# Kernel optimization log

Hardware: AMD Instinct MI355X
Metric: run time of the kernel (lower is better)

## Reference

```python
import jax, jax.numpy as jnp
import numpy as np

BN_EPS = 1e-5

def _batchnorm(x):
    # BatchNorm1d(affine=False) in training mode: per-feature batch stats, biased var
    m = jnp.mean(x, axis=0)
    v = jnp.var(x, axis=0)
    return (x - m) * jax.lax.rsqrt(v + BN_EPS)

def setup_inputs() -> dict:
    key = jax.random.key(0)
    ks = jax.random.split(key, 8)
    B, S, H, I = 2, 2048, 1024, 4096
    NE, NS, K = 16384, 128, 16
    return {
        "hidden_states": jax.random.normal(ks[0], (B, S, H), dtype=jnp.float32),
        "gate_w": jax.random.normal(ks[1], (I, H), dtype=jnp.float32) * 0.02,
        "up_w": jax.random.normal(ks[2], (I, H), dtype=jnp.float32) * 0.02,
        "down_w": jax.random.normal(ks[3], (H, I), dtype=jnp.float32) * 0.02,
        "router_x_w": jax.random.normal(ks[4], (NS, H), dtype=jnp.float32) * 0.02,
        "router_y_w": jax.random.normal(ks[5], (NS, H), dtype=jnp.float32) * 0.02,
        "up_embed": jax.random.normal(ks[6], (NE, H), dtype=jnp.float32) * 0.02,
        "down_embed": jax.random.normal(ks[7], (NE, H), dtype=jnp.float32) * 0.02,
        "top_k": K,
    }

def reference(hidden_states, gate_w, up_w, down_w, router_x_w, router_y_w, up_embed, down_embed, top_k):
    B, S, H = hidden_states.shape
    ns = router_x_w.shape[0]  # num_expert_sqrt
    x = hidden_states.reshape(-1, H)  # [N, H], N = B*S

    # product-key router: two grid log-softmaxes, outer-sum, global top-k
    lpx = jax.nn.log_softmax(_batchnorm(x @ router_x_w.T), axis=-1)  # [N, ns]
    lpy = jax.nn.log_softmax(_batchnorm(x @ router_y_w.T), axis=-1)  # [N, ns]
    all_scores = (lpx[:, :, None] + lpy[:, None, :]).reshape(-1, ns * ns)  # [N, ns^2]
    scores, indices = jax.lax.top_k(all_scores, top_k)  # [N, k]
    routing_weights = jnp.exp(scores)

    # per-token expert embedding gather + small bmm chain (PEER-style)
    ue = up_embed[indices]    # [N, k, H]
    de = down_embed[indices]  # [N, k, H]
    ew = jnp.einsum('nkh,nh->nk', ue, x)
    ew = jax.nn.silu(ew) * routing_weights
    experts_states = jnp.einsum('nk,nkh->nh', ew, de).reshape(B, S, H)

    # dense gated MLP
    dense = (jax.nn.silu(x @ gate_w.T) * (x @ up_w.T)) @ down_w.T
    return dense.reshape(B, S, H) + experts_states
```

## Files before the change

kernel.cpp:

```cpp
#include <hip/hip_runtime.h>

typedef float f32x4 __attribute__((ext_vector_type(4)));
typedef short bf16x8 __attribute__((ext_vector_type(8)));
typedef unsigned short u16;

#define NEG_INF (-1e30f)

__device__ __forceinline__ u16 f2bf(float f) {
    unsigned u = __builtin_bit_cast(unsigned, f);
    unsigned r = u + 0x7FFFu + ((u >> 16) & 1u);
    return (u16)(r >> 16);
}
__device__ __forceinline__ unsigned pk2(float a, float b) {
    unsigned r;
    asm("v_cvt_pk_bf16_f32 %0, %1, %2" : "=v"(r) : "v"(a), "v"(b));
    return r;
}

__device__ __forceinline__ float wave_max(float v) {
    #pragma unroll
    for (int o = 32; o > 0; o >>= 1) v = fmaxf(v, __shfl_xor(v, o, 64));
    return v;
}
__device__ __forceinline__ float wave_sum(float v) {
    #pragma unroll
    for (int o = 32; o > 0; o >>= 1) v += __shfl_xor(v, o, 64);
    return v;
}
__device__ __forceinline__ void wave_argmax(float& v, int& i) {
    #pragma unroll
    for (int o = 32; o > 0; o >>= 1) {
        float ov = __shfl_xor(v, o, 64);
        int oi = __shfl_xor(i, o, 64);
        if (ov > v || (ov == v && oi < i)) { v = ov; i = oi; }
    }
}

__device__ __forceinline__ void g2l16(const void* g, void* l) {
    __builtin_amdgcn_global_load_lds((__attribute__((address_space(1))) void*)g,
                                     (__attribute__((address_space(3))) void*)l,
                                     16, 0, 0);
}

template<int NROUND>
__device__ __forceinline__ void stage_bf16(const u16* __restrict__ src, int ld,
                                           u16* dst, int tid) {
    #pragma unroll
    for (int r = 0; r < NROUND; ++r) {
        int e = r * 2048 + tid * 8;
        int row = e >> 6, col = e & 63;
        g2l16(src + (size_t)row * ld + col, dst + e);
    }
}
template<int NROUND>
__device__ __forceinline__ void stage_f32(const float* __restrict__ src, int ld,
                                          u16* dst, int tid) {
    #pragma unroll
    for (int r = 0; r < NROUND; ++r) {
        int e = r * 2048 + tid * 8;
        int row = e >> 6, col = e & 63;
        const float* s = src + (size_t)row * ld + col;
        float4 a = *reinterpret_cast<const float4*>(s);
        float4 b = *reinterpret_cast<const float4*>(s + 4);
        uint4 pk;
        pk.x = pk2(a.x, a.y); pk.y = pk2(a.z, a.w);
        pk.z = pk2(b.x, b.y); pk.w = pk2(b.z, b.w);
        *reinterpret_cast<uint4*>(dst + e) = pk;
    }
}
__device__ __forceinline__ bf16x8 frag(const u16* lds, int row0, int ks, int lane) {
    return *reinterpret_cast<const bf16x8*>(
        lds + (row0 + (lane & 15)) * 64 + ks * 32 + (lane >> 4) * 8);
}

template<int NROUND>
__device__ __forceinline__ void stage32_bf16(const u16* __restrict__ src, int ld,
                                             u16* dst, int tid) {
    #pragma unroll
    for (int r = 0; r < NROUND; ++r) {
        int e = r * 2048 + tid * 8;
        int row = e >> 5, col = e & 31;
        g2l16(src + (size_t)row * ld + col, dst + e);
    }
}
template<int NROUND>
__device__ __forceinline__ void stage32_f32(const float* __restrict__ src, int ld,
                                            u16* dst, int tid) {
    #pragma unroll
    for (int r = 0; r < NROUND; ++r) {
        int e = r * 1024 + tid * 4;
        int row = e >> 5, col = e & 31;
        float4 v = *reinterpret_cast<const float4*>(src + (size_t)row * ld + col);
        uint2 pk;
        pk.x = pk2(v.x, v.y); pk.y = pk2(v.z, v.w);
        *reinterpret_cast<uint2*>(dst + e) = pk;
    }
}
__device__ __forceinline__ bf16x8 frag32(const u16* lds, int row0, int lane) {
    return *reinterpret_cast<const bf16x8*>(
        lds + (row0 + (lane & 15)) * 32 + (lane >> 4) * 8);
}

__global__ void conv_x(const float* __restrict__ s, u16* __restrict__ d) {
    size_t i = (size_t)blockIdx.x * 256 + threadIdx.x;
    float4 v = *reinterpret_cast<const float4*>(s + i * 4);
    uint2 pk;
    pk.x = pk2(v.x, v.y); pk.y = pk2(v.z, v.w);
    *reinterpret_cast<uint2*>(d + i * 4) = pk;
}

__global__ __launch_bounds__(256, 2) void gemm_router(
    const float* __restrict__ X, const float* __restrict__ RX, const float* __restrict__ RY,
    float* __restrict__ R) {
    __shared__ u16 As[8192];
    __shared__ u16 Bs[4096];
    int tid = threadIdx.x, lane = tid & 63, wave = tid >> 6;
    int rowBase = blockIdx.y * 128, colBase = blockIdx.x * 64;
    const float* Bp = (blockIdx.x < 2) ? RX + (size_t)colBase * 1024
                                       : RY + (size_t)(colBase - 128) * 1024;
    int wm = (wave >> 1) * 64, wn = (wave & 1) * 32;
    f32x4 acc[4][2] = {};
    for (int k0 = 0; k0 < 1024; k0 += 64) {
        stage_f32<4>(X + (size_t)rowBase * 1024 + k0, 1024, As, tid);
        stage_f32<2>(Bp + k0, 1024, Bs, tid);
        __syncthreads();
        #pragma unroll
        for (int ks = 0; ks < 2; ++ks) {
            bf16x8 af[4], bfr[2];
            #pragma unroll
            for (int i = 0; i < 4; ++i) af[i] = frag(As, wm + i * 16, ks, lane);
            #pragma unroll
            for (int j = 0; j < 2; ++j) bfr[j] = frag(Bs, wn + j * 16, ks, lane);
            #pragma unroll
            for (int i = 0; i < 4; ++i)
                #pragma unroll
                for (int j = 0; j < 2; ++j)
                    acc[i][j] = __builtin_amdgcn_mfma_f32_16x16x32_bf16(af[i], bfr[j], acc[i][j], 0, 0, 0);
        }
        __syncthreads();
    }
    int rq = (lane >> 4) * 4, cq = lane & 15;
    #pragma unroll
    for (int i = 0; i < 4; ++i)
        #pragma unroll
        for (int j = 0; j < 2; ++j) {
            int col = colBase + wn + j * 16 + cq;
            #pragma unroll
            for (int r = 0; r < 4; ++r) {
                int row = rowBase + wm + i * 16 + rq + r;
                R[(size_t)row * 256 + col] = acc[i][j][r];
            }
        }
}

template<bool ABF>
__global__ __launch_bounds__(256, 2) void gemm_gateup(
    const float* __restrict__ Xf, const u16* __restrict__ Xb,
    const float* __restrict__ GW, const float* __restrict__ UW,
    u16* __restrict__ H2) {
    __shared__ u16 As[4096];
    __shared__ u16 Gs[4096];
    __shared__ u16 Us[4096];
    int tid = threadIdx.x, lane = tid & 63, wave = tid >> 6;
    int b = blockIdx.x;
    int xcd = b & 7, ii = b >> 3;
    int by = xcd * 4 + (ii >> 5), bx = ii & 31;
    int rowBase = by * 128, colBase = bx * 128;
    int wm = (wave >> 1) * 64, wn = (wave & 1) * 64;
    f32x4 accg[4][4] = {}, accu[4][4] = {};
    for (int k0 = 0; k0 < 1024; k0 += 32) {
        if constexpr (ABF) stage32_bf16<2>(Xb + (size_t)rowBase * 1024 + k0, 1024, As, tid);
        else               stage32_f32<4>(Xf + (size_t)rowBase * 1024 + k0, 1024, As, tid);
        stage32_f32<4>(GW + (size_t)colBase * 1024 + k0, 1024, Gs, tid);
        stage32_f32<4>(UW + (size_t)colBase * 1024 + k0, 1024, Us, tid);
        __syncthreads();
        bf16x8 gf[4], uf[4];
        #pragma unroll
        for (int j = 0; j < 4; ++j) { gf[j] = frag32(Gs, wn + j * 16, lane);
                                      uf[j] = frag32(Us, wn + j * 16, lane); }
        #pragma unroll
        for (int i = 0; i < 4; ++i) {
            bf16x8 af = frag32(As, wm + i * 16, lane);
            #pragma unroll
            for (int j = 0; j < 4; ++j) {
                accg[i][j] = __builtin_amdgcn_mfma_f32_16x16x32_bf16(af, gf[j], accg[i][j], 0, 0, 0);
                accu[i][j] = __builtin_amdgcn_mfma_f32_16x16x32_bf16(af, uf[j], accu[i][j], 0, 0, 0);
            }
        }
        __syncthreads();
    }
    int rq = (lane >> 4) * 4, cq = lane & 15;
    #pragma unroll
    for (int i = 0; i < 4; ++i)
        #pragma unroll
        for (int j = 0; j < 4; ++j) {
            int col = colBase + wn + j * 16 + cq;
            #pragma unroll
            for (int r = 0; r < 4; ++r) {
                int row = rowBase + wm + i * 16 + rq + r;
                float gv = accg[i][j][r], uv = accu[i][j][r];
                float h = (gv / (1.f + __expf(-gv))) * uv;
                H2[(size_t)row * 4096 + col] = f2bf(h);
            }
        }
}

__global__ __launch_bounds__(256, 2) void gemm_down_add(
    const u16* __restrict__ H2, const float* __restrict__ DW, float* __restrict__ Out) {
    __shared__ u16 As[8192];
    __shared__ u16 Bs[4096];
    int b = blockIdx.x, tid = threadIdx.x;
    int xcd = b & 7, ii = b >> 3;
    int by = xcd * 4 + (ii >> 4), bx = ii & 15;
    int lane = tid & 63, wave = tid >> 6;
    int rowBase = by * 128, colBase = bx * 64;
    int wm = (wave >> 1) * 64, wn = (wave & 1) * 32;
    f32x4 acc[4][2] = {};
    for (int k0 = 0; k0 < 4096; k0 += 64) {
        stage_bf16<4>(H2 + (size_t)rowBase * 4096 + k0, 4096, As, tid);
        stage_f32<2>(DW + (size_t)colBase * 4096 + k0, 4096, Bs, tid);
        __syncthreads();
        #pragma unroll
        for (int ks = 0; ks < 2; ++ks) {
            bf16x8 af[4], bfr[2];
            #pragma unroll
            for (int i2 = 0; i2 < 4; ++i2) af[i2] = frag(As, wm + i2 * 16, ks, lane);
            #pragma unroll
            for (int j = 0; j < 2; ++j) bfr[j] = frag(Bs, wn + j * 16, ks, lane);
            #pragma unroll
            for (int i2 = 0; i2 < 4; ++i2)
                #pragma unroll
                for (int j = 0; j < 2; ++j)
                    acc[i2][j] = __builtin_amdgcn_mfma_f32_16x16x32_bf16(af[i2], bfr[j], acc[i2][j], 0, 0, 0);
        }
        __syncthreads();
    }
    int rq = (lane >> 4) * 4, cq = lane & 15;
    #pragma unroll
    for (int i2 = 0; i2 < 4; ++i2)
        #pragma unroll
        for (int j = 0; j < 2; ++j) {
            int col = colBase + wn + j * 16 + cq;
            #pragma unroll
            for (int r = 0; r < 4; ++r) {
                int row = rowBase + wm + i2 * 16 + rq + r;
                size_t o = (size_t)row * 1024 + col;
                Out[o] = acc[i2][j][r] + Out[o];
            }
        }
}

__global__ __launch_bounds__(256) void expert_store(
    const float* __restrict__ X, const float* __restrict__ UE, const float* __restrict__ DE,
    const int* __restrict__ idxs, const float* __restrict__ wts, float* __restrict__ Out) {
    int n = blockIdx.x, tid = threadIdx.x;
    int lane = tid & 63, wave = tid >> 6;
    __shared__ float xs[1024];
    __shared__ float ews[16];
    __shared__ int sidx[16];
    __shared__ float swt[16];
    if (tid < 16) {
        sidx[tid] = min(max(idxs[n * 16 + tid], 0), 16383);
        swt[tid] = wts[n * 16 + tid];
    }
    {
        float4 v = reinterpret_cast<const float4*>(X + (size_t)n * 1024)[tid];
        *reinterpret_cast<float4*>(xs + tid * 4) = v;
    }
    __syncthreads();
    #pragma unroll
    for (int q = 0; q < 4; ++q) {
        int e = wave * 4 + q;
        const float* row = UE + (size_t)sidx[e] * 1024;
        float acc = 0.f;
        #pragma unroll
        for (int c = 0; c < 4; ++c) {
            int h = c * 256 + lane * 4;
            float4 a = *reinterpret_cast<const float4*>(row + h);
            float4 xv = *reinterpret_cast<const float4*>(xs + h);
            acc += a.x * xv.x + a.y * xv.y + a.z * xv.z + a.w * xv.w;
        }
        acc = wave_sum(acc);
        if (lane == 0) {
            float s = acc / (1.f + __expf(-acc));
            ews[e] = s * swt[e];
        }
    }
    __syncthreads();
    float4 a = make_float4(0.f, 0.f, 0.f, 0.f);
    int h = tid * 4;
    #pragma unroll
    for (int e = 0; e < 16; ++e) {
        const float* row = DE + (size_t)sidx[e] * 1024;
        float4 v = *reinterpret_cast<const float4*>(row + h);
        float w = ews[e];
        a.x += w * v.x; a.y += w * v.y;
        a.z += w * v.z; a.w += w * v.w;
    }
    reinterpret_cast<float4*>(Out + (size_t)n * 1024)[tid] = a;
}

__global__ void bn_stats(const float* __restrict__ R, float* __restrict__ stats) {
    int c = threadIdx.x;
    int r0 = blockIdx.x * 64;
    float s = 0.f, s2 = 0.f;
    for (int r = r0; r < r0 + 64; ++r) {
        float v = R[(size_t)r * 256 + c];
        s += v; s2 += v * v;
    }
    atomicAdd(&stats[c], s);
    atomicAdd(&stats[256 + c], s2);
}

__global__ __launch_bounds__(64) void router_topk(
    const float* __restrict__ R, const float* __restrict__ stats,
    int* __restrict__ idx_out, float* __restrict__ wt_out) {
    int n = blockIdx.x, lane = threadIdx.x;
    const float invN = 1.0f / 4096.0f;
    float z[4];
    #pragma unroll
    for (int p = 0; p < 4; ++p) {
        int c = p * 64 + lane;
        float mean = stats[c] * invN;
        float var = fmaxf(stats[256 + c] * invN - mean * mean, 0.f);
        float v = R[(size_t)n * 256 + c];
        z[p] = (v - mean) * rsqrtf(var + 1e-5f);
    }
    float mx = wave_max(fmaxf(z[0], z[1]));
    float sx = __logf(wave_sum(__expf(z[0] - mx) + __expf(z[1] - mx)));
    float lx0 = z[0] - mx - sx, lx1 = z[1] - mx - sx;
    float my = wave_max(fmaxf(z[2], z[3]));
    float sy = __logf(wave_sum(__expf(z[2] - my) + __expf(z[3] - my)));
    float ly0 = z[2] - my - sy, ly1 = z[3] - my - sy;

    __shared__ float tx[16], ty[16];
    __shared__ int txc[16], tyc[16];
    float v0 = lx0, v1 = lx1;
    for (int t = 0; t < 16; ++t) {
        float bv; int bc;
        if (v1 > v0) { bv = v1; bc = lane + 64; } else { bv = v0; bc = lane; }
        wave_argmax(bv, bc);
        if (lane == 0) { tx[t] = bv; txc[t] = bc; }
        if (bc == lane) v0 = NEG_INF;
        else if (bc == lane + 64) v1 = NEG_INF;
    }
    v0 = ly0; v1 = ly1;
    for (int t = 0; t < 16; ++t) {
        float bv; int bc;
        if (v1 > v0) { bv = v1; bc = lane + 64; } else { bv = v0; bc = lane; }
        wave_argmax(bv, bc);
        if (lane == 0) { ty[t] = bv; tyc[t] = bc; }
        if (bc == lane) v0 = NEG_INF;
        else if (bc == lane + 64) v1 = NEG_INF;
    }
    __syncthreads();
    float cv[4]; int ci[4];
    #pragma unroll
    for (int p = 0; p < 4; ++p) {
        int pid = p * 64 + lane;
        cv[p] = tx[pid >> 4] + ty[pid & 15];
        ci[p] = pid;
    }
    for (int t = 0; t < 16; ++t) {
        float bv = cv[0]; int bc = ci[0];
        #pragma unroll
        for (int p = 1; p < 4; ++p)
            if (cv[p] > bv) { bv = cv[p]; bc = ci[p]; }
        wave_argmax(bv, bc);
        if (lane == 0) {
            idx_out[n * 16 + t] = txc[bc >> 4] * 128 + tyc[bc & 15];
            wt_out[n * 16 + t] = __expf(bv);
        }
        #pragma unroll
        for (int p = 0; p < 4; ++p)
            if (ci[p] == bc) cv[p] = NEG_INF;
    }
}

extern "C" void kernel_launch(void* const* d_in, const int* in_sizes, int n_in,
                              void* d_out, int out_size, void* d_ws, size_t ws_size,
                              hipStream_t stream) {
    const float* x   = (const float*)d_in[0];
    const float* gw  = (const float*)d_in[1];
    const float* uw  = (const float*)d_in[2];
    const float* dw  = (const float*)d_in[3];
    const float* rxw = (const float*)d_in[4];
    const float* ryw = (const float*)d_in[5];
    const float* ue  = (const float*)d_in[6];
    const float* de  = (const float*)d_in[7];
    float* out = (float*)d_out;

    char* p = (char*)d_ws;
    float* stats = (float*)p; p += 16384;
    int*   idxb  = (int*)p;   p += 262144;
    float* wtb   = (float*)p; p += 262144;
    float* R     = (float*)p;
    u16*   H2    = (u16*)p;

    bool useXb = ws_size >= 42483712ull;
    u16* xb = (u16*)((char*)d_ws + 34095104ull);

    hipMemsetAsync(stats, 0, 512 * sizeof(float), stream);
    if (useXb) conv_x<<<4096, 256, 0, stream>>>(x, xb);

    gemm_router<<<dim3(4, 32), 256, 0, stream>>>(x, rxw, ryw, R);
    bn_stats<<<64, 256, 0, stream>>>(R, stats);
    router_topk<<<4096, 64, 0, stream>>>(R, stats, idxb, wtb);
    expert_store<<<4096, 256, 0, stream>>>(x, ue, de, idxb, wtb, out);

    if (useXb) gemm_gateup<true ><<<1024, 256, 0, stream>>>(nullptr, xb, gw, uw, H2);
    else       gemm_gateup<false><<<1024, 256, 0, stream>>>(x, nullptr, gw, uw, H2);
    gemm_down_add<<<512, 256, 0, stream>>>(H2, dw, out);
}
```

Measured before the change: 546.0 us.

## Double-buffer and swizzle LDS tiles in all three GEMMs

Adds LDS double buffering to the router, gate/up and down GEMMs. Global loads for the next k-tile are issued before the current tile's MFMAs, and the fp32-to-bf16 conversion is written to LDS afterwards, so each step needs one barrier instead of two. LDS layouts get an XOR swizzle meant to avoid bank conflicts on the fragment reads. The router now uses 64-row tiles and can read pre-converted bf16 X, and the down GEMM moves to 512 threads with smaller per-wave tiles. The cost is twice the LDS and more registers for the prefetched fp32 data, which may reduce occupancy.

```diff
diff --git a/kernel.cpp b/kernel.cpp
--- a/kernel.cpp
+++ b/kernel.cpp
@@ -41,64 +41,83 @@
                                      (__attribute__((address_space(3))) void*)l,
                                      16, 0, 0);
 }
-
-template<int NROUND>
-__device__ __forceinline__ void stage_bf16(const u16* __restrict__ src, int ld,
-                                           u16* dst, int tid) {
-    #pragma unroll
-    for (int r = 0; r < NROUND; ++r) {
+__device__ __forceinline__ int swz8(int row, int c) { return c ^ (row & 7); }
+__device__ __forceinline__ int swz4(int row, int c) { return c ^ ((row >> 1) & 3); }
+
+template<int NTHR>
+__device__ __forceinline__ void stageA64(const u16* __restrict__ src, int ld,
+                                         u16* dst, int tid) {
+    #pragma unroll
+    for (int r = 0; r < 2; ++r) {
+        int e = r * NTHR * 8 + tid * 8;
+        int row = e >> 6, c = (e >> 3) & 7;
+        g2l16(src + (size_t)row * ld + swz8(row, c) * 8, dst + e);
+    }
+}
+__device__ __forceinline__ void stageA32(const u16* __restrict__ src, int ld,
+                                         u16* dst, int tid) {
+    #pragma unroll
+    for (int r = 0; r < 2; ++r) {
         int e = r * 2048 + tid * 8;
-        int row = e >> 6, col = e & 63;
-        g2l16(src + (size_t)row * ld + col, dst + e);
-    }
-}
-template<int NROUND>
-__device__ __forceinline__ void stage_f32(const float* __restrict__ src, int ld,
-                                          u16* dst, int tid) {
-    #pragma unroll
-    for (int r = 0; r < NROUND; ++r) {
-        int e = r * 2048 + tid * 8;
-        int row = e >> 6, col = e & 63;
-        const float* s = src + (size_t)row * ld + col;
-        float4 a = *reinterpret_cast<const float4*>(s);
-        float4 b = *reinterpret_cast<const float4*>(s + 4);
-        uint4 pk;
-        pk.x = pk2(a.x, a.y); pk.y = pk2(a.z, a.w);
-        pk.z = pk2(b.x, b.y); pk.w = pk2(b.z, b.w);
-        *reinterpret_cast<uint4*>(dst + e) = pk;
-    }
-}
-__device__ __forceinline__ bf16x8 frag(const u16* lds, int row0, int ks, int lane) {
-    return *reinterpret_cast<const bf16x8*>(
-        lds + (row0 + (lane & 15)) * 64 + ks * 32 + (lane >> 4) * 8);
-}
-
-template<int NROUND>
-__device__ __forceinline__ void stage32_bf16(const u16* __restrict__ src, int ld,
-                                             u16* dst, int tid) {
-    #pragma unroll
-    for (int r = 0; r < NROUND; ++r) {
-        int e = r * 2048 + tid * 8;
-        int row = e >> 5, col = e & 31;
-        g2l16(src + (size_t)row * ld + col, dst + e);
-    }
-}
-template<int NROUND>
-__device__ __forceinline__ void stage32_f32(const float* __restrict__ src, int ld,
-                                            u16* dst, int tid) {
-    #pragma unroll
-    for (int r = 0; r < NROUND; ++r) {
-        int e = r * 1024 + tid * 4;
-        int row = e >> 5, col = e & 31;
-        float4 v = *reinterpret_cast<const float4*>(src + (size_t)row * ld + col);
-        uint2 pk;
-        pk.x = pk2(v.x, v.y); pk.y = pk2(v.z, v.w);
-        *reinterpret_cast<uint2*>(dst + e) = pk;
-    }
-}
-__device__ __forceinline__ bf16x8 frag32(const u16* lds, int row0, int lane) {
-    return *reinterpret_cast<const bf16x8*>(
-        lds + (row0 + (lane & 15)) * 32 + (lane >> 4) * 8);
+        int row = e >> 5, c = (e >> 3) & 3;
+        g2l16(src + (size_t)row * ld + swz4(row, c) * 8, dst + e);
+    }
+}
+
+__device__ __forceinline__ void loadT64_256(const float* __restrict__ src, int ld,
+                                            int tid, float4* v) {
+    int row = tid >> 2, col = (tid & 3) * 16;
+    const float* s = src + (size_t)row * ld + col;
+    v[0] = *reinterpret_cast<const float4*>(s);
+    v[1] = *reinterpret_cast<const float4*>(s + 4);
+    v[2] = *reinterpret_cast<const float4*>(s + 8);
+    v[3] = *reinterpret_cast<const float4*>(s + 12);
+}
+__device__ __forceinline__ void writeT64_256(const float4* v, u16* dst, int tid) {
+    int row = tid >> 2, c0 = (tid & 3) * 2;
+    uint4 p0 = { pk2(v[0].x, v[0].y), pk2(v[0].z, v[0].w), pk2(v[1].x, v[1].y), pk2(v[1].z, v[1].w) };
+    uint4 p1 = { pk2(v[2].x, v[2].y), pk2(v[2].z, v[2].w), pk2(v[3].x, v[3].y), pk2(v[3].z, v[3].w) };
+    *reinterpret_cast<uint4*>(dst + row * 64 + swz8(row, c0) * 8) = p0;
+    *reinterpret_cast<uint4*>(dst + row * 64 + swz8(row, c0 + 1) * 8) = p1;
+}
+__device__ __forceinline__ void loadT64_512(const float* __restrict__ src, int ld,
+                                            int tid, float4* v) {
+    int row = tid >> 3, col = (tid & 7) * 8;
+    const float* s = src + (size_t)row * ld + col;
+    v[0] = *reinterpret_cast<const float4*>(s);
+    v[1] = *reinterpret_cast<const float4*>(s + 4);
+}
+__device__ __forceinline__ void writeT64_512(const float4* v, u16* dst, int tid) {
+    int row = tid >> 3, c = tid & 7;
+    uint4 p = { pk2(v[0].x, v[0].y), pk2(v[0].z, v[0].w), pk2(v[1].x, v[1].y), pk2(v[1].z, v[1].w) };
+    *reinterpret_cast<uint4*>(dst + row * 64 + swz8(row, c) * 8) = p;
+}
+__device__ __forceinline__ void loadT32(const float* __restrict__ src, int ld,
+                                        int tid, float4* v) {
+    int row = tid >> 1, col = (tid & 1) * 16;
+    const float* s = src + (size_t)row * ld + col;
+    v[0] = *reinterpret_cast<const float4*>(s);
+    v[1] = *reinterpret_cast<const float4*>(s + 4);
+    v[2] = *reinterpret_cast<const float4*>(s + 8);
+    v[3] = *reinterpret_cast<const float4*>(s + 12);
+}
+__device__ __forceinline__ void writeT32(const float4* v, u16* dst, int tid) {
+    int row = tid >> 1, c0 = (tid & 1) * 2;
+    uint4 p0 = { pk2(v[0].x, v[0].y), pk2(v[0].z, v[0].w), pk2(v[1].x, v[1].y), pk2(v[1].z, v[1].w) };
+    uint4 p1 = { pk2(v[2].x, v[2].y), pk2(v[2].z, v[2].w), pk2(v[3].x, v[3].y), pk2(v[3].z, v[3].w) };
+    *reinterpret_cast<uint4*>(dst + row * 32 + swz4(row, c0) * 8) = p0;
+    *reinterpret_cast<uint4*>(dst + row * 32 + swz4(row, c0 + 1) * 8) = p1;
+}
+
+__device__ __forceinline__ bf16x8 frag64s(const u16* lds, int row0, int ks, int lane) {
+    int row = row0 + (lane & 15);
+    int c = ks * 4 + (lane >> 4);
+    return *reinterpret_cast<const bf16x8*>(lds + row * 64 + swz8(row, c) * 8);
+}
+__device__ __forceinline__ bf16x8 frag32s(const u16* lds, int row0, int lane) {
+    int row = row0 + (lane & 15);
+    int c = lane >> 4;
+    return *reinterpret_cast<const bf16x8*>(lds + row * 32 + swz4(row, c) * 8);
 }
 
 __global__ void conv_x(const float* __restrict__ s, u16* __restrict__ d) {
@@ -109,39 +128,57 @@
     *reinterpret_cast<uint2*>(d + i * 4) = pk;
 }
 
+template<bool ABF>
 __global__ __launch_bounds__(256, 2) void gemm_router(
-    const float* __restrict__ X, const float* __restrict__ RX, const float* __restrict__ RY,
+    const float* __restrict__ Xf, const u16* __restrict__ Xb,
+    const float* __restrict__ RX, const float* __restrict__ RY,
     float* __restrict__ R) {
-    __shared__ u16 As[8192];
-    __shared__ u16 Bs[4096];
+    __shared__ __align__(16) u16 As[2][4096];
+    __shared__ __align__(16) u16 Bs[2][4096];
     int tid = threadIdx.x, lane = tid & 63, wave = tid >> 6;
-    int rowBase = blockIdx.y * 128, colBase = blockIdx.x * 64;
+    int rowBase = blockIdx.y * 64, colBase = blockIdx.x * 64;
     const float* Bp = (blockIdx.x < 2) ? RX + (size_t)colBase * 1024
                                        : RY + (size_t)(colBase - 128) * 1024;
-    int wm = (wave >> 1) * 64, wn = (wave & 1) * 32;
-    f32x4 acc[4][2] = {};
-    for (int k0 = 0; k0 < 1024; k0 += 64) {
-        stage_f32<4>(X + (size_t)rowBase * 1024 + k0, 1024, As, tid);
-        stage_f32<2>(Bp + k0, 1024, Bs, tid);
-        __syncthreads();
+    int wm = (wave >> 1) * 32, wn = (wave & 1) * 32;
+    f32x4 acc[2][2] = {};
+    float4 av[4], bv[4];
+    if constexpr (ABF) stageA64<256>(Xb + (size_t)rowBase * 1024, 1024, As[0], tid);
+    else               { loadT64_256(Xf + (size_t)rowBase * 1024, 1024, tid, av);
+                         writeT64_256(av, As[0], tid); }
+    loadT64_256(Bp, 1024, tid, bv);
+    writeT64_256(bv, Bs[0], tid);
+    __syncthreads();
+    int cur = 0;
+    for (int t = 0; t < 16; ++t) {
+        if (t < 15) {
+            int k0 = (t + 1) * 64;
+            if constexpr (ABF) stageA64<256>(Xb + (size_t)rowBase * 1024 + k0, 1024, As[cur ^ 1], tid);
+            else               loadT64_256(Xf + (size_t)rowBase * 1024 + k0, 1024, tid, av);
+            loadT64_256(Bp + k0, 1024, tid, bv);
+        }
         #pragma unroll
         for (int ks = 0; ks < 2; ++ks) {
-            bf16x8 af[4], bfr[2];
-            #pragma unroll
-            for (int i = 0; i < 4; ++i) af[i] = frag(As, wm + i * 16, ks, lane);
-            #pragma unroll
-            for (int j = 0; j < 2; ++j) bfr[j] = frag(Bs, wn + j * 16, ks, lane);
-            #pragma unroll
-            for (int i = 0; i < 4; ++i)
+            bf16x8 af[2], bfr[2];
+            #pragma unroll
+            for (int i = 0; i < 2; ++i) af[i] = frag64s(As[cur], wm + i * 16, ks, lane);
+            #pragma unroll
+            for (int j = 0; j < 2; ++j) bfr[j] = frag64s(Bs[cur], wn + j * 16, ks, lane);
+            #pragma unroll
+            for (int i = 0; i < 2; ++i)
                 #pragma unroll
                 for (int j = 0; j < 2; ++j)
                     acc[i][j] = __builtin_amdgcn_mfma_f32_16x16x32_bf16(af[i], bfr[j], acc[i][j], 0, 0, 0);
         }
+        if (t < 15) {
+            if constexpr (!ABF) writeT64_256(av, As[cur ^ 1], tid);
+            writeT64_256(bv, Bs[cur ^ 1], tid);
+        }
         __syncthreads();
+        cur ^= 1;
     }
     int rq = (lane >> 4) * 4, cq = lane & 15;
     #pragma unroll
-    for (int i = 0; i < 4; ++i)
+    for (int i = 0; i < 2; ++i)
         #pragma unroll
         for (int j = 0; j < 2; ++j) {
             int col = colBase + wn + j * 16 + cq;
@@ -158,36 +195,55 @@
     const float* __restrict__ Xf, const u16* __restrict__ Xb,
     const float* __restrict__ GW, const float* __restrict__ UW,
     u16* __restrict__ H2) {
-    __shared__ u16 As[4096];
-    __shared__ u16 Gs[4096];
-    __shared__ u16 Us[4096];
+    __shared__ __align__(16) u16 As[2][4096];
+    __shared__ __align__(16) u16 Gs[2][4096];
+    __shared__ __align__(16) u16 Us[2][4096];
     int tid = threadIdx.x, lane = tid & 63, wave = tid >> 6;
-    int b = blockIdx.x;
-    int xcd = b & 7, ii = b >> 3;
+    int b = blockIdx.x, xcd = b & 7, ii = b >> 3;
     int by = xcd * 4 + (ii >> 5), bx = ii & 31;
     int rowBase = by * 128, colBase = bx * 128;
+    const float* Gp = GW + (size_t)colBase * 1024;
+    const float* Up = UW + (size_t)colBase * 1024;
     int wm = (wave >> 1) * 64, wn = (wave & 1) * 64;
     f32x4 accg[4][4] = {}, accu[4][4] = {};
-    for (int k0 = 0; k0 < 1024; k0 += 32) {
-        if constexpr (ABF) stage32_bf16<2>(Xb + (size_t)rowBase * 1024 + k0, 1024, As, tid);
-        else               stage32_f32<4>(Xf + (size_t)rowBase * 1024 + k0, 1024, As, tid);
-        stage32_f32<4>(GW + (size_t)colBase * 1024 + k0, 1024, Gs, tid);
-        stage32_f32<4>(UW + (size_t)colBase * 1024 + k0, 1024, Us, tid);
-        __syncthreads();
+    float4 av[4], gv[4], uv[4];
+    if constexpr (ABF) stageA32(Xb + (size_t)rowBase * 1024, 1024, As[0], tid);
+    else               { loadT32(Xf + (size_t)rowBase * 1024, 1024, tid, av);
+                         writeT32(av, As[0], tid); }
+    loadT32(Gp, 1024, tid, gv);
+    loadT32(Up, 1024, tid, uv);
+    writeT32(gv, Gs[0], tid);
+    writeT32(uv, Us[0], tid);
+    __syncthreads();
+    int cur = 0;
+    for (int t = 0; t < 32; ++t) {
+        if (t < 31) {
+            int k0 = (t + 1) * 32;
+            if constexpr (ABF) stageA32(Xb + (size_t)rowBase * 1024 + k0, 1024, As[cur ^ 1], tid);
+            else               loadT32(Xf + (size_t)rowBase * 1024 + k0, 1024, tid, av);
+            loadT32(Gp + k0, 1024, tid, gv);
+            loadT32(Up + k0, 1024, tid, uv);
+        }
         bf16x8 gf[4], uf[4];
         #pragma unroll
-        for (int j = 0; j < 4; ++j) { gf[j] = frag32(Gs, wn + j * 16, lane);
-                                      uf[j] = frag32(Us, wn + j * 16, lane); }
+        for (int j = 0; j < 4; ++j) { gf[j] = frag32s(Gs[cur], wn + j * 16, lane);
+                                      uf[j] = frag32s(Us[cur], wn + j * 16, lane); }
         #pragma unroll
         for (int i = 0; i < 4; ++i) {
-            bf16x8 af = frag32(As, wm + i * 16, lane);
+            bf16x8 af = frag32s(As[cur], wm + i * 16, lane);
             #pragma unroll
             for (int j = 0; j < 4; ++j) {
                 accg[i][j] = __builtin_amdgcn_mfma_f32_16x16x32_bf16(af, gf[j], accg[i][j], 0, 0, 0);
                 accu[i][j] = __builtin_amdgcn_mfma_f32_16x16x32_bf16(af, uf[j], accu[i][j], 0, 0, 0);
             }
         }
+        if (t < 31) {
+            if constexpr (!ABF) writeT32(av, As[cur ^ 1], tid);
+            writeT32(gv, Gs[cur ^ 1], tid);
+            writeT32(uv, Us[cur ^ 1], tid);
+        }
         __syncthreads();
+        cur ^= 1;
     }
     int rq = (lane >> 4) * 4, cq = lane & 15;
     #pragma unroll
@@ -198,54 +254,65 @@
             #pragma unroll
             for (int r = 0; r < 4; ++r) {
                 int row = rowBase + wm + i * 16 + rq + r;
-                float gv = accg[i][j][r], uv = accu[i][j][r];
-                float h = (gv / (1.f + __expf(-gv))) * uv;
+                float gvv = accg[i][j][r], uvv = accu[i][j][r];
+                float h = (gvv / (1.f + __expf(-gvv))) * uvv;
                 H2[(size_t)row * 4096 + col] = f2bf(h);
             }
         }
 }
 
-__global__ __launch_bounds__(256, 2) void gemm_down_add(
+__global__ __launch_bounds__(512, 4) void gemm_down_pipe(
     const u16* __restrict__ H2, const float* __restrict__ DW, float* __restrict__ Out) {
-    __shared__ u16 As[8192];
-    __shared__ u16 Bs[4096];
-    int b = blockIdx.x, tid = threadIdx.x;
-    int xcd = b & 7, ii = b >> 3;
+    __shared__ __align__(16) u16 As[2][8192];
+    __shared__ __align__(16) u16 Bs[2][4096];
+    int tid = threadIdx.x, lane = tid & 63, wave = tid >> 6;
+    int b = blockIdx.x, xcd = b & 7, ii = b >> 3;
     int by = xcd * 4 + (ii >> 4), bx = ii & 15;
-    int lane = tid & 63, wave = tid >> 6;
     int rowBase = by * 128, colBase = bx * 64;
-    int wm = (wave >> 1) * 64, wn = (wave & 1) * 32;
-    f32x4 acc[4][2] = {};
-    for (int k0 = 0; k0 < 4096; k0 += 64) {
-        stage_bf16<4>(H2 + (size_t)rowBase * 4096 + k0, 4096, As, tid);
-        stage_f32<2>(DW + (size_t)colBase * 4096 + k0, 4096, Bs, tid);
-        __syncthreads();
+    const u16* Ap = H2 + (size_t)rowBase * 4096;
+    const float* Bp = DW + (size_t)colBase * 4096;
+    int wm = (wave >> 1) * 32, wn = (wave & 1) * 32;
+    f32x4 acc[2][2] = {};
+    float4 bv[2];
+    stageA64<512>(Ap, 4096, As[0], tid);
+    loadT64_512(Bp, 4096, tid, bv);
+    writeT64_512(bv, Bs[0], tid);
+    __syncthreads();
+    int cur = 0;
+    for (int t = 0; t < 64; ++t) {
+        if (t < 63) {
+            int k0 = (t + 1) * 64;
+            stageA64<512>(Ap + k0, 4096, As[cur ^ 1], tid);
+            loadT64_512(Bp + k0, 4096, tid, bv);
+        }
         #pragma unroll
         for (int ks = 0; ks < 2; ++ks) {
-            bf16x8 af[4], bfr[2];
-            #pragma unroll
-            for (int i2 = 0; i2 < 4; ++i2) af[i2] = frag(As, wm + i2 * 16, ks, lane);
-            #pragma unroll
-            for (int j = 0; j < 2; ++j) bfr[j] = frag(Bs, wn + j * 16, ks, lane);
-            #pragma unroll
-            for (int i2 = 0; i2 < 4; ++i2)
+            bf16x8 af[2], bfr[2];
+            #pragma unroll
+            for (int i = 0; i < 2; ++i) af[i] = frag64s(As[cur], wm + i * 16, ks, lane);
+            #pragma unroll
+            for (int j = 0; j < 2; ++j) bfr[j] = frag64s(Bs[cur], wn + j * 16, ks, lane);
+            #pragma unroll
+            for (int i = 0; i < 2; ++i)
                 #pragma unroll
                 for (int j = 0; j < 2; ++j)
-                    acc[i2][j] = __builtin_amdgcn_mfma_f32_16x16x32_bf16(af[i2], bfr[j], acc[i2][j], 0, 0, 0);
-        }
+                    acc[i][j] = __builtin_amdgcn_mfma_f32_16x16x32_bf16(af[i], bfr[j], acc[i][j], 0, 0, 0);
+        }
+        if (t < 63) writeT64_512(bv, Bs[cur ^ 1], tid);
         __syncthreads();
+        cur ^= 1;
     }
     int rq = (lane >> 4) * 4, cq = lane & 15;
     #pragma unroll
-    for (int i2 = 0; i2 < 4; ++i2)
+    for (int i = 0; i < 2; ++i)
         #pragma unroll
         for (int j = 0; j < 2; ++j) {
             int col = colBase + wn + j * 16 + cq;
             #pragma unroll
             for (int r = 0; r < 4; ++r) {
-                int row = rowBase + wm + i2 * 16 + rq + r;
+                int row = rowBase + wm + i * 16 + rq + r;
                 size_t o = (size_t)row * 1024 + col;
-                Out[o] = acc[i2][j][r] + Out[o];
+                Out[o] = acc[i][j][r] + Out[o];
             }
         }
 }
@@ -403,12 +470,13 @@
     hipMemsetAsync(stats, 0, 512 * sizeof(float), stream);
     if (useXb) conv_x<<<4096, 256, 0, stream>>>(x, xb);
 
-    gemm_router<<<dim3(4, 32), 256, 0, stream>>>(x, rxw, ryw, R);
+    if (useXb) gemm_router<true ><<<dim3(4, 64), 256, 0, stream>>>(x, xb, rxw, ryw, R);
+    else       gemm_router<false><<<dim3(4, 64), 256, 0, stream>>>(x, (const u16*)x, rxw, ryw, R);
     bn_stats<<<64, 256, 0, stream>>>(R, stats);
     router_topk<<<4096, 64, 0, stream>>>(R, stats, idxb, wtb);
     expert_store<<<4096, 256, 0, stream>>>(x, ue, de, idxb, wtb, out);
 
-    if (useXb) gemm_gateup<true ><<<1024, 256, 0, stream>>>(nullptr, xb, gw, uw, H2);
-    else       gemm_gateup<false><<<1024, 256, 0, stream>>>(x, nullptr, gw, uw, H2);
-    gemm_down_add<<<512, 256, 0, stream>>>(H2, dw, out);
-}
+    if (useXb) gemm_gateup<true ><<<1024, 256, 0, stream>>>(x, xb, gw, uw, H2);
+    else       gemm_gateup<false><<<1024, 256, 0, stream>>>(x, (const u16*)x, gw, uw, H2);
+    gemm_down_pipe<<<512, 512, 0, stream>>>(H2, dw, out);
+}
```

New measurement: 515.9 us. -5.5%, faster.
